# Kernel tuning notes

Hardware: AMD Instinct MI355X
Metric: run time of the kernel (lower is better)

The kernel has to match this reference:

```python
import jax, jax.numpy as jnp
import numpy as np
import math

N_HEAD = 16
N_EMBD = 2048

def setup_inputs() -> dict:
    key = jax.random.key(0)
    k1, k2, k3, k4, k5 = jax.random.split(key, 5)
    B, T, C = 4, 2048, N_EMBD
    x = jax.random.normal(k1, (B, T, C), dtype=jnp.float32)
    # torch Linear stores weight [out,in]; we store [in,out] for x @ W
    s_attn = 1.0 / math.sqrt(C)
    w_attn = jax.random.normal(k2, (C, 3 * C), dtype=jnp.float32) * s_attn
    b_attn = jnp.zeros((3 * C,), dtype=jnp.float32)
    w_proj = jax.random.normal(k3, (C, C), dtype=jnp.float32) * s_attn
    b_proj = jnp.zeros((C,), dtype=jnp.float32)
    return {"x": x, "w_attn": w_attn, "b_attn": b_attn,
            "w_proj": w_proj, "b_proj": b_proj}

def reference(x, w_attn, b_attn, w_proj, b_proj):
    B, T, C = x.shape
    H = N_HEAD
    D = C // H
    qkv = x @ w_attn + b_attn                      # [B,T,3C]
    q, k, v = jnp.split(qkv, 3, axis=2)
    q = q.reshape(B, T, H, D).transpose(0, 2, 1, 3)  # [B,H,T,D]
    k = k.reshape(B, T, H, D).transpose(0, 2, 1, 3)
    v = v.reshape(B, T, H, D).transpose(0, 2, 1, 3)
    scale = 1.0 / math.sqrt(D)
    att = jnp.einsum('bhqd,bhkd->bhqk', q, k) * scale  # [B,H,T,T]
    causal = jnp.tril(jnp.ones((T, T), dtype=bool))    # mask slice bias[:, :, FULL_T-T:FULL_T, :FULL_T] with FULL_T==T
    att = jnp.where(causal[None, None], att, -jnp.inf)
    att = jax.nn.softmax(att.astype(jnp.float32), axis=-1).astype(att.dtype)
    y = jnp.einsum('bhqk,bhkd->bhqd', att, v)          # [B,H,T,D]
    y = y.transpose(0, 2, 1, 3).reshape(B, T, C)
    return y @ w_proj + b_proj
```

## Files before the change

kernel.cpp:

```cpp
#include <hip/hip_runtime.h>
#include <hip/hip_bf16.h>

#define NB 4
#define TT 2048
#define CC 2048
#define HH 16
#define DD 128

typedef short bvec8 __attribute__((ext_vector_type(8)));
typedef float fvec4 __attribute__((ext_vector_type(4)));

__device__ __forceinline__ void gload16(const void* g, void* l) {
  __builtin_amdgcn_global_load_lds(
      (__attribute__((address_space(1))) void*)g,
      (__attribute__((address_space(3))) void*)l, 16, 0, 0);
}

__device__ __forceinline__ unsigned short f2bf(float f) {
  union { float f; unsigned int u; } x; x.f = f;
  unsigned int u = x.u;
  return (unsigned short)((u + 0x7FFFu + ((u >> 16) & 1u)) >> 16);
}

__device__ __forceinline__ fvec4 mfma16(bvec8 a, bvec8 b, fvec4 c) {
  return __builtin_amdgcn_mfma_f32_16x16x32_bf16(a, b, c, 0, 0, 0);
}

#define KSC (0.08838834764831845f * 1.4426950408889634f)

__global__ __launch_bounds__(256) void k_cvt(const float* __restrict__ in,
                                             unsigned short* __restrict__ out, int n4) {
  int i = blockIdx.x * 256 + threadIdx.x;
  if (i >= n4) return;
  float4 v = ((const float4*)in)[i];
  ushort4 o;
  o.x = f2bf(v.x); o.y = f2bf(v.y); o.z = f2bf(v.z); o.w = f2bf(v.w);
  ((ushort4*)out)[i] = o;
}

__global__ __launch_bounds__(256) void k_transpose(const float* __restrict__ in,
                                                   unsigned short* __restrict__ out,
                                                   int R, int Cn) {
  __shared__ unsigned short tile[64][65];
  int tC = blockIdx.x * 64, tR = blockIdx.y * 64;
  int t = threadIdx.x;
  for (int i = 0; i < 16; i++) {
    int idx = t + i * 256; int r = idx >> 6, c = idx & 63;
    tile[r][c] = f2bf(in[(size_t)(tR + r) * Cn + tC + c]);
  }
  __syncthreads();
  for (int i = 0; i < 16; i++) {
    int idx = t + i * 256; int r = idx >> 6, c = idx & 63;
    out[(size_t)(tC + r) * R + tR + c] = tile[c][r];
  }
}

template <int EPI>
__global__ __launch_bounds__(512, 2) void k_gemm8(
    const unsigned short* __restrict__ A,
    const unsigned short* __restrict__ Bt,
    const float* __restrict__ bias,
    unsigned short* __restrict__ qk,
    unsigned short* __restrict__ vt,
    float* __restrict__ out) {
  const int K = CC;
  const int nt = K / 64;
  __shared__ unsigned short sm[2][32768];

  int tid = threadIdx.x;
  int wid = tid >> 6, ln = tid & 63, gl = ln >> 4, lo = ln & 15;
  int wr = wid >> 2, wc = wid & 3;

  unsigned nx = gridDim.x;
  unsigned orig = blockIdx.y * nx + blockIdx.x;
  unsigned cpx = (nx * gridDim.y) >> 3;
  unsigned wg = (orig & 7) * cpx + (orig >> 3);
  int m0 = (int)(wg / nx) * 256, n0 = (int)(wg % nx) * 256;

  auto stageA = [&](int buf, int half, int kt) {
#pragma unroll
    for (int j = 0; j < 2; j++) {
      int c = j * 512 + tid;
      int r = c >> 3;
      int kc = (c & 7) ^ (r & 7);
      gload16(A + (size_t)(m0 + half * 128 + r) * K + kt * 64 + kc * 8,
              &sm[buf][(size_t)(half * 1024 + c) * 8]);
    }
  };
  auto stageB = [&](int buf, int half, int kt) {
#pragma unroll
    for (int j = 0; j < 2; j++) {
      int c = j * 512 + tid;
      int r = c >> 3;
      int kc = (c & 7) ^ (r & 7);
      gload16(Bt + (size_t)(n0 + half * 128 + r) * K + kt * 64 + kc * 8,
              &sm[buf][16384 + (size_t)(half * 1024 + c) * 8]);
    }
  };

#define AFRAG(buf, mi, ks) \
  (*(const bvec8*)&sm[buf][(((wr * 128 + (mi) * 16 + lo) * 8) + ((((ks) * 4 + gl)) ^ (lo & 7))) * 8])
#define BFRAG(buf, nj, ks) \
  (*(const bvec8*)&sm[buf][16384 + (((wc * 64 + (nj) * 16 + lo) * 8) + ((((ks) * 4 + gl)) ^ (lo & 7))) * 8])

  fvec4 acc[8][4];
  fvec4 zero = {0.f, 0.f, 0.f, 0.f};
#pragma unroll
  for (int i = 0; i < 8; i++)
#pragma unroll
    for (int j = 0; j < 4; j++) acc[i][j] = zero;

  stageA(0, 0, 0); stageA(0, 1, 0); stageB(0, 0, 0); stageB(0, 1, 0);
  stageA(1, 0, 1); stageA(1, 1, 1); stageB(1, 0, 1); stageB(1, 1, 1);

  for (int t = 0; t < nt; t++) {
    int cur = t & 1;
    bvec8 a0[4], a1[4], a2[4], a3[4], b0[4], b1[4];

    if (t + 1 < nt) {
      asm volatile("s_waitcnt vmcnt(8)" ::: "memory");
    } else {
      asm volatile("s_waitcnt vmcnt(0)" ::: "memory");
    }
    __builtin_amdgcn_sched_barrier(0);
    __builtin_amdgcn_s_barrier();
    __builtin_amdgcn_sched_barrier(0);

#pragma unroll
    for (int mi = 0; mi < 4; mi++) a0[mi] = AFRAG(cur, mi, 0);
#pragma unroll
    for (int nj = 0; nj < 4; nj++) b0[nj] = BFRAG(cur, nj, 0);
#pragma unroll
    for (int mi = 0; mi < 4; mi++) a1[mi] = AFRAG(cur, mi + 4, 0);
#pragma unroll
    for (int mi = 0; mi < 4; mi++) a2[mi] = AFRAG(cur, mi, 1);
#pragma unroll
    for (int nj = 0; nj < 4; nj++) b1[nj] = BFRAG(cur, nj, 1);
    __builtin_amdgcn_sched_barrier(0);

    __builtin_amdgcn_s_setprio(1);
#pragma unroll
    for (int mi = 0; mi < 4; mi++)
#pragma unroll
      for (int nj = 0; nj < 4; nj++) acc[mi][nj] = mfma16(a0[mi], b0[nj], acc[mi][nj]);
    __builtin_amdgcn_s_setprio(0);

#pragma unroll
    for (int mi = 0; mi < 4; mi++) a3[mi] = AFRAG(cur, mi + 4, 1);
    __builtin_amdgcn_sched_barrier(0);

    __builtin_amdgcn_s_setprio(1);
#pragma unroll
    for (int mi = 0; mi < 4; mi++)
#pragma unroll
      for (int nj = 0; nj < 4; nj++) acc[mi + 4][nj] = mfma16(a1[mi], b0[nj], acc[mi + 4][nj]);
    __builtin_amdgcn_s_setprio(0);

    __builtin_amdgcn_s_setprio(1);
#pragma unroll
    for (int mi = 0; mi < 4; mi++)
#pragma unroll
      for (int nj = 0; nj < 4; nj++) acc[mi][nj] = mfma16(a2[mi], b1[nj], acc[mi][nj]);
    __builtin_amdgcn_s_setprio(0);

    asm volatile("s_waitcnt lgkmcnt(0)" ::: "memory");
    __builtin_amdgcn_sched_barrier(0);
    __builtin_amdgcn_s_barrier();
    if (t + 2 < nt) {
      stageA(cur, 0, t + 2); stageA(cur, 1, t + 2);
      stageB(cur, 0, t + 2); stageB(cur, 1, t + 2);
    }

    __builtin_amdgcn_s_setprio(1);
#pragma unroll
    for (int mi = 0; mi < 4; mi++)
#pragma unroll
      for (int nj = 0; nj < 4; nj++) acc[mi + 4][nj] = mfma16(a3[mi], b1[nj], acc[mi + 4][nj]);
    __builtin_amdgcn_s_setprio(0);
  }

  if (EPI == 0) {
#pragma unroll
    for (int nj = 0; nj < 4; nj++) {
      int n = n0 + wc * 64 + nj * 16 + lo;
      float bn = bias[n];
      int s = n >> 11, hh = (n >> 7) & 15, d = n & 127;
      float mulv = (s == 1) ? KSC : 1.0f;
#pragma unroll
      for (int mi = 0; mi < 8; mi++) {
        int mb = m0 + wr * 128 + mi * 16 + gl * 4;
        int b = mb >> 11, t0 = mb & 2047;
        if (s < 2) {
          size_t base = ((((size_t)s * NB + b) * HH + hh) * TT) * DD;
#pragma unroll
          for (int r = 0; r < 4; r++)
            qk[base + (size_t)(t0 + r) * DD + d] = f2bf((acc[mi][nj][r] + bn) * mulv);
        } else {
          size_t base = ((((size_t)b * HH + hh) * (TT / 8) + (t0 >> 3)) * DD + d) * 8 + (t0 & 7);
          ushort4 o;
          o.x = f2bf(acc[mi][nj][0] + bn);
          o.y = f2bf(acc[mi][nj][1] + bn);
          o.z = f2bf(acc[mi][nj][2] + bn);
          o.w = f2bf(acc[mi][nj][3] + bn);
          *(ushort4*)&vt[base] = o;
        }
      }
    }
  } else {
#pragma unroll
    for (int nj = 0; nj < 4; nj++) {
      int n = n0 + wc * 64 + nj * 16 + lo;
      float bn = bias[n];
#pragma unroll
      for (int mi = 0; mi < 8; mi++) {
        int m = m0 + wr * 128 + mi * 16 + gl * 4;
#pragma unroll
        for (int r = 0; r < 4; r++) out[(size_t)(m + r) * CC + n] = acc[mi][nj][r] + bn;
      }
    }
  }
#undef AFRAG
#undef BFRAG
}

__global__ __launch_bounds__(256, 2) void k_attn(
    const unsigned short* __restrict__ qk,
    const unsigned short* __restrict__ vt,
    unsigned short* __restrict__ yb) {
  __shared__ unsigned short Ks[2][8192];
  __shared__ unsigned short Vs[2][8192];
  __shared__ unsigned short Ps[4][2048];
  int tid = threadIdx.x, wid = tid >> 6, ln = tid & 63;
  int gl = ln >> 4, lo = ln & 15;
  int qp = blockIdx.x & 7;
  int bh = blockIdx.x >> 3;
  int b = bh >> 4, h = bh & 15;
  const unsigned short* Q  = qk + (((size_t)b * HH + h) * TT) * DD;
  const unsigned short* Kg = qk + ((((size_t)NB + b) * HH + h) * TT) * DD;
  const unsigned short* Vg = vt + (((size_t)b * HH + h) * (TT / 8)) * DD * 8;
  fvec4 zero = {0.f, 0.f, 0.f, 0.f};

  auto stageK = [&](int buf, int it) {
    int k0 = it * 64;
#pragma unroll
    for (int j = 0; j < 4; j++) {
      int c = j * 256 + tid;
      int r = c >> 4, cc = c & 15;
      gload16(Kg + (size_t)(k0 + r) * DD + ((cc ^ (r & 7)) * 8), &Ks[buf][(j * 256 + wid * 64) * 8]);
    }
  };
  auto stageV = [&](int buf, int it) {
    int k0 = it * 64;
#pragma unroll
    for (int j = 0; j < 4; j++) {
      int c = j * 256 + tid;
      int cc = c >> 7, d = c & 127;
      gload16(Vg + ((size_t)(k0 / 8 + cc) * DD + d) * 8, &Vs[buf][(j * 256 + wid * 64) * 8]);
    }
  };

  auto smax = [&](fvec4 (&sa)[4], float (&mr)[4], float (&lr)[4], fvec4 (&oa)[8],
                  int q0m, int k0, bool domask, int psoff) {
    float p[4][4], mxl[4];
#pragma unroll
    for (int r = 0; r < 4; r++) {
      int qrow = q0m + gl * 4 + r;
      float m = -1e30f;
      if (domask) {
#pragma unroll
        for (int fn = 0; fn < 4; fn++) {
          int kkg = k0 + fn * 16 + lo;
          float v = (kkg <= qrow) ? sa[fn][r] : -1e30f;
          p[fn][r] = v; m = fmaxf(m, v);
        }
      } else {
#pragma unroll
        for (int fn = 0; fn < 4; fn++) {
          float v = sa[fn][r];
          p[fn][r] = v; m = fmaxf(m, v);
        }
      }
      mxl[r] = m;
    }
    bool c = (mxl[0] > mr[0] + 8.f) || (mxl[1] > mr[1] + 8.f) ||
             (mxl[2] > mr[2] + 8.f) || (mxl[3] > mr[3] + 8.f);
    if (__any(c)) {
#pragma unroll
      for (int r = 0; r < 4; r++) {
        float m = mxl[r];
#pragma unroll
        for (int dlt = 1; dlt < 16; dlt <<= 1) m = fmaxf(m, __shfl_xor(m, dlt));
        float mnew = fmaxf(mr[r], m);
        float corr = exp2f(mr[r] - mnew);
        mr[r] = mnew; lr[r] *= corr;
#pragma unroll
        for (int fd = 0; fd < 8; fd++) oa[fd][r] *= corr;
      }
    }
#pragma unroll
    for (int r = 0; r < 4; r++)
#pragma unroll
      for (int fn = 0; fn < 4; fn++) {
        float pv = exp2f(p[fn][r] - mr[r]);
        p[fn][r] = pv; lr[r] += pv;
      }
#pragma unroll
    for (int fn = 0; fn < 4; fn++)
#pragma unroll
      for (int r = 0; r < 4; r++) {
        int qr = gl * 4 + r;
        int kc = fn * 16 + lo;
        Ps[wid][psoff + (qr * 8 + ((kc >> 3) ^ (qr & 7))) * 8 + (kc & 7)] = f2bf(p[fn][r]);
      }
  };

  for (int pass = 0; pass < 2; pass++) {
    int qt = pass ? (15 - qp) : qp;
    int q0w = qt * 128 + wid * 32;

    bvec8 qf0[4], qf1[4];
#pragma unroll
    for (int ks = 0; ks < 4; ks++) {
      qf0[ks] = *(const bvec8*)(Q + (size_t)(q0w + lo) * DD + ks * 32 + gl * 8);
      qf1[ks] = *(const bvec8*)(Q + (size_t)(q0w + 16 + lo) * DD + ks * 32 + gl * 8);
    }

    fvec4 oacc0[8], oacc1[8];
#pragma unroll
    for (int i = 0; i < 8; i++) { oacc0[i] = zero; oacc1[i] = zero; }
    float mr0[4] = {-1e30f, -1e30f, -1e30f, -1e30f};
    float mr1[4] = {-1e30f, -1e30f, -1e30f, -1e30f};
    float lr0[4] = {0.f, 0.f, 0.f, 0.f};
    float lr1[4] = {0.f, 0.f, 0.f, 0.f};

    int ntiles = 2 * qt + 2;
    stageK(0, 0); stageV(0, 0);
    asm volatile("s_waitcnt vmcnt(8)" ::: "memory");
    __builtin_amdgcn_sched_barrier(0);
    __builtin_amdgcn_s_barrier();
    __builtin_amdgcn_sched_barrier(0);

    for (int it = 0; it < ntiles; it++) {
      int cur = it & 1;
      int k0 = it * 64;
      bool more = (it + 1 < ntiles);
      if (more) { stageK(cur ^ 1, it + 1); stageV(cur ^ 1, it + 1); }

      fvec4 sa0[4], sa1[4];
#pragma unroll
      for (int fn = 0; fn < 4; fn++) {
        fvec4 s0 = zero, s1 = zero;
#pragma unroll
        for (int ks = 0; ks < 4; ks++) {
          int r = fn * 16 + lo;
          int cd = ks * 4 + gl;
          bvec8 kf = *(const bvec8*)&Ks[cur][(r * 16 + (cd ^ (r & 7))) * 8];
          s0 = mfma16(qf0[ks], kf, s0);
          s1 = mfma16(qf1[ks], kf, s1);
        }
        sa0[fn] = s0; sa1[fn] = s1;
      }

      smax(sa0, mr0, lr0, oacc0, q0w,      k0, (k0 + 63) > q0w,        0);
      smax(sa1, mr1, lr1, oacc1, q0w + 16, k0, (k0 + 63) > (q0w + 16), 1024);

      if (more) {
        asm volatile("s_waitcnt vmcnt(16)" ::: "memory");
      } else {
        asm volatile("s_waitcnt vmcnt(0)" ::: "memory");
      }
      __builtin_amdgcn_sched_barrier(0);
      __builtin_amdgcn_s_barrier();
      __builtin_amdgcn_sched_barrier(0);

#pragma unroll
      for (int ks2 = 0; ks2 < 2; ks2++) {
        bvec8 pf0 = *(const bvec8*)&Ps[wid][(lo * 8 + ((ks2 * 4 + gl) ^ (lo & 7))) * 8];
        bvec8 pf1 = *(const bvec8*)&Ps[wid][1024 + (lo * 8 + ((ks2 * 4 + gl) ^ (lo & 7))) * 8];
#pragma unroll
        for (int fd = 0; fd < 8; fd++) {
          bvec8 vf = *(const bvec8*)&Vs[cur][((ks2 * 4 + gl) * 128 + fd * 16 + lo) * 8];
          oacc0[fd] = mfma16(pf0, vf, oacc0[fd]);
          oacc1[fd] = mfma16(pf1, vf, oacc1[fd]);
        }
      }

      if (more) {
        asm volatile("s_waitcnt vmcnt(8)" ::: "memory");
      } else {
        asm volatile("s_waitcnt vmcnt(0)" ::: "memory");
      }
      __builtin_amdgcn_sched_barrier(0);
      __builtin_amdgcn_s_barrier();
      __builtin_amdgcn_sched_barrier(0);
    }

#pragma unroll
    for (int r = 0; r < 4; r++) {
      float l0 = lr0[r], l1 = lr1[r];
#pragma unroll
      for (int dlt = 1; dlt < 16; dlt <<= 1) {
        l0 += __shfl_xor(l0, dlt);
        l1 += __shfl_xor(l1, dlt);
      }
      int qrow0 = q0w + gl * 4 + r;
      int qrow1 = q0w + 16 + gl * 4 + r;
      float inv0 = 1.f / l0, inv1 = 1.f / l1;
#pragma unroll
      for (int fd = 0; fd < 8; fd++) {
        int d = fd * 16 + lo;
        yb[((size_t)b * TT + qrow0) * CC + h * DD + d] = f2bf(oacc0[fd][r] * inv0);
        yb[((size_t)b * TT + qrow1) * CC + h * DD + d] = f2bf(oacc1[fd][r] * inv1);
      }
    }
  }
}

extern "C" void kernel_launch(void* const* d_in, const int* in_sizes, int n_in,
                              void* d_out, int out_size, void* d_ws, size_t ws_size,
                              hipStream_t stream) {
  const float* x      = (const float*)d_in[0];
  const float* w_attn = (const float*)d_in[1];
  const float* b_attn = (const float*)d_in[2];
  const float* w_proj = (const float*)d_in[3];
  const float* b_proj = (const float*)d_in[4];
  float* out = (float*)d_out;

  char* ws = (char*)d_ws;
  unsigned short* xb    = (unsigned short*)(ws);
  unsigned short* wab_t = (unsigned short*)(ws + 33554432);
  unsigned short* wpb_t = (unsigned short*)(ws + 58720256);
  unsigned short* qkws  = (unsigned short*)(ws + 67108864);
  unsigned short* vtws  = (unsigned short*)(ws + 134217728);
  unsigned short* ybws  = (unsigned short*)(ws + 167772160);

  hipLaunchKernelGGL(k_cvt, dim3(16384), dim3(256), 0, stream, x, xb, 4194304);
  hipLaunchKernelGGL(k_transpose, dim3(96, 32), dim3(256), 0, stream, w_attn, wab_t, 2048, 6144);
  hipLaunchKernelGGL(k_transpose, dim3(32, 32), dim3(256), 0, stream, w_proj, wpb_t, 2048, 2048);
  hipLaunchKernelGGL((k_gemm8<0>), dim3(24, 32), dim3(512), 0, stream,
                     xb, wab_t, b_attn, qkws, vtws, (float*)nullptr);
  hipLaunchKernelGGL(k_attn, dim3(512), dim3(256), 0, stream, qkws, vtws, ybws);
  hipLaunchKernelGGL((k_gemm8<1>), dim3(8, 32), dim3(512), 0, stream,
                     ybws, wpb_t, b_proj, (unsigned short*)nullptr, (unsigned short*)nullptr, out);
}
```

Baseline: 444.0 us.

## Restage GEMM B prefetch, stage Q/K epilogue through LDS, remap tile and attention block order

The GEMM now issues the B-tile loads for the next k-step mid-iteration into the other buffer instead of two steps ahead, adjusting the vmcnt wait to match. The tile-to-workgroup mapping becomes column-major, and the Q/K epilogue writes results into swizzled shared memory first, then emits coalesced 16-byte global stores instead of scattered 2-byte stores. The attention kernel interleaves query-chunk and batch-head order so consecutive blocks share a query position across heads. The goal is better store coalescing and cache locality, at the cost of a shallower B prefetch that may expose load latency.

```diff
diff --git a/kernel.cpp b/kernel.cpp
--- a/kernel.cpp
+++ b/kernel.cpp
@@ -71,11 +71,12 @@
   int wid = tid >> 6, ln = tid & 63, gl = ln >> 4, lo = ln & 15;
   int wr = wid >> 2, wc = wid & 3;
 
-  unsigned nx = gridDim.x;
-  unsigned orig = blockIdx.y * nx + blockIdx.x;
-  unsigned cpx = (nx * gridDim.y) >> 3;
-  unsigned wg = (orig & 7) * cpx + (orig >> 3);
-  int m0 = (int)(wg / nx) * 256, n0 = (int)(wg % nx) * 256;
+  unsigned gx = gridDim.x, gy = gridDim.y;
+  unsigned orig = blockIdx.y * gx + blockIdx.x;
+  unsigned cpx = (gx * gy) >> 3;
+  unsigned wg2 = (orig & 7) * cpx + (orig >> 3);
+  int n0 = (int)(wg2 / gy) * 256;
+  int m0 = (int)(wg2 % gy) * 256;
 
   auto stageA = [&](int buf, int half, int kt) {
 #pragma unroll
@@ -111,14 +112,14 @@
     for (int j = 0; j < 4; j++) acc[i][j] = zero;
 
   stageA(0, 0, 0); stageA(0, 1, 0); stageB(0, 0, 0); stageB(0, 1, 0);
-  stageA(1, 0, 1); stageA(1, 1, 1); stageB(1, 0, 1); stageB(1, 1, 1);
+  stageA(1, 0, 1); stageA(1, 1, 1);
 
   for (int t = 0; t < nt; t++) {
     int cur = t & 1;
     bvec8 a0[4], a1[4], a2[4], a3[4], b0[4], b1[4];
 
     if (t + 1 < nt) {
-      asm volatile("s_waitcnt vmcnt(8)" ::: "memory");
+      asm volatile("s_waitcnt vmcnt(4)" ::: "memory");
     } else {
       asm volatile("s_waitcnt vmcnt(0)" ::: "memory");
     }
@@ -136,6 +137,7 @@
     for (int mi = 0; mi < 4; mi++) a2[mi] = AFRAG(cur, mi, 1);
 #pragma unroll
     for (int nj = 0; nj < 4; nj++) b1[nj] = BFRAG(cur, nj, 1);
+    if (t + 1 < nt) { stageB(cur ^ 1, 0, t + 1); stageB(cur ^ 1, 1, t + 1); }
     __builtin_amdgcn_sched_barrier(0);
 
     __builtin_amdgcn_s_setprio(1);
@@ -166,10 +168,7 @@
     asm volatile("s_waitcnt lgkmcnt(0)" ::: "memory");
     __builtin_amdgcn_sched_barrier(0);
     __builtin_amdgcn_s_barrier();
-    if (t + 2 < nt) {
-      stageA(cur, 0, t + 2); stageA(cur, 1, t + 2);
-      stageB(cur, 0, t + 2); stageB(cur, 1, t + 2);
-    }
+    if (t + 2 < nt) { stageA(cur, 0, t + 2); stageA(cur, 1, t + 2); }
 
     __builtin_amdgcn_s_setprio(1);
 #pragma unroll
@@ -180,22 +179,49 @@
   }
 
   if (EPI == 0) {
-#pragma unroll
-    for (int nj = 0; nj < 4; nj++) {
-      int n = n0 + wc * 64 + nj * 16 + lo;
-      float bn = bias[n];
-      int s = n >> 11, hh = (n >> 7) & 15, d = n & 127;
+    int s = n0 >> 11;
+    if (s < 2) {
+      unsigned short* se = (unsigned short*)sm;
       float mulv = (s == 1) ? KSC : 1.0f;
 #pragma unroll
-      for (int mi = 0; mi < 8; mi++) {
-        int mb = m0 + wr * 128 + mi * 16 + gl * 4;
+      for (int nj = 0; nj < 4; nj++) {
+        int coln = wc * 64 + nj * 16 + lo;
+        float bn = bias[n0 + coln];
+#pragma unroll
+        for (int mi = 0; mi < 8; mi++) {
+          int rowbase = wr * 128 + mi * 16 + gl * 4;
+#pragma unroll
+          for (int r = 0; r < 4; r++) {
+            int row = rowbase + r;
+            int colsw = coln ^ (((row >> 2) & 7) << 3);
+            se[row * 256 + colsw] = f2bf((acc[mi][nj][r] + bn) * mulv);
+          }
+        }
+      }
+      __syncthreads();
+#pragma unroll
+      for (int k = 0; k < 16; k++) {
+        int c = k * 512 + tid;
+        int row = c >> 5, cpos = c & 31;
+        int cposw = cpos ^ ((row >> 2) & 7);
+        bvec8 v = *(const bvec8*)&se[row * 256 + cposw * 8];
+        int mb = m0 + row;
         int b = mb >> 11, t0 = mb & 2047;
-        if (s < 2) {
-          size_t base = ((((size_t)s * NB + b) * HH + hh) * TT) * DD;
-#pragma unroll
-          for (int r = 0; r < 4; r++)
-            qk[base + (size_t)(t0 + r) * DD + d] = f2bf((acc[mi][nj][r] + bn) * mulv);
-        } else {
+        int col = cpos * 8;
+        int hh = ((n0 + col) >> 7) & 15;
+        int d = col & 127;
+        *(bvec8*)&qk[((((size_t)s * NB + b) * HH + hh) * TT + t0) * DD + d] = v;
+      }
+    } else {
+#pragma unroll
+      for (int nj = 0; nj < 4; nj++) {
+        int n = n0 + wc * 64 + nj * 16 + lo;
+        float bn = bias[n];
+        int hh = (n >> 7) & 15, d = n & 127;
+#pragma unroll
+        for (int mi = 0; mi < 8; mi++) {
+          int mb = m0 + wr * 128 + mi * 16 + gl * 4;
+          int b = mb >> 11, t0 = mb & 2047;
           size_t base = ((((size_t)b * HH + hh) * (TT / 8) + (t0 >> 3)) * DD + d) * 8 + (t0 & 7);
           ushort4 o;
           o.x = f2bf(acc[mi][nj][0] + bn);
@@ -232,8 +258,8 @@
   __shared__ unsigned short Ps[4][2048];
   int tid = threadIdx.x, wid = tid >> 6, ln = tid & 63;
   int gl = ln >> 4, lo = ln & 15;
-  int qp = blockIdx.x & 7;
-  int bh = blockIdx.x >> 3;
+  int qp = blockIdx.x >> 6;
+  int bh = blockIdx.x & 63;
   int b = bh >> 4, h = bh & 15;
   const unsigned short* Q  = qk + (((size_t)b * HH + h) * TT) * DD;
   const unsigned short* Kg = qk + ((((size_t)NB + b) * HH + h) * TT) * DD;
```

Result: no change. 446.6 us (+0.6%).
